# Optimization experiments

Hardware: AMD Instinct MI355X
Metric: run time of the kernel (lower is better)

The kernel has to match this reference:

```python
import jax, jax.numpy as jnp
import numpy as np

GRID_SIZE = 4
ORDER = 3
NUM_BASIS = GRID_SIZE + ORDER  # 7
KNOTS = jnp.linspace(-1.0, 1.0, NUM_BASIS + ORDER + 1)  # 11 knots


def _normalise(x):
    # eval-mode with uninitialized running stats: use batch min/max
    min_val = x.min(axis=0)
    max_val = x.max(axis=0)
    width = jnp.maximum(max_val - min_val, 0.01)
    centre = 0.5 * (max_val + min_val)
    scaled = (x - centre) / (0.5 * width)
    return jnp.clip(scaled, -2.0, 2.0)


def _bspline_basis(x):
    # x: (B, I) -> basis: (B, I, NUM_BASIS), de Boor recursion vectorized over i
    xe = x[..., None]  # (B, I, 1)
    idx = jnp.arange(NUM_BASIS)
    left, right = KNOTS[idx], KNOTS[idx + 1]
    basis = ((xe >= left) & (xe < right)).astype(x.dtype)
    last = jnp.where(xe[..., 0] == KNOTS[NUM_BASIS], 1.0, basis[..., -1])
    basis = basis.at[..., -1].set(last)
    for k in range(1, ORDER + 1):
        d1 = KNOTS[idx + k] - KNOTS[idx]
        d2 = KNOTS[idx + k + 1] - KNOTS[idx + 1]
        b_next = jnp.concatenate([basis[..., 1:], jnp.zeros_like(basis[..., :1])], axis=-1)
        t1 = jnp.where(d1 > 0, (xe - KNOTS[idx]) / jnp.where(d1 > 0, d1, 1.0), 0.0) * basis
        t2 = jnp.where(d2 > 0, (KNOTS[idx + k + 1] - xe) / jnp.where(d2 > 0, d2, 1.0), 0.0) * b_next
        basis = t1 + t2
    return basis


def setup_inputs() -> dict:
    key = jax.random.key(0)
    k1, k2, k3 = jax.random.split(key, 3)
    B, I, O = 8192, 256, 256
    x = jax.random.normal(k1, (B, I), dtype=jnp.float32)
    # xavier-uniform base_weight
    bound = float(np.sqrt(6.0 / (I + O)))
    base_weight = jax.random.uniform(k2, (O, I), minval=-bound, maxval=bound, dtype=jnp.float32)
    spline_weight = jnp.ones((O, I), dtype=jnp.float32)
    spline_coeff = 0.001 * jax.random.normal(k3, (O, I, NUM_BASIS), dtype=jnp.float32)
    bias = jnp.zeros((O,), dtype=jnp.float32)
    return {"x": x, "base_weight": base_weight, "spline_weight": spline_weight,
            "spline_coeff": spline_coeff, "bias": bias}


def reference(x, base_weight, spline_weight, spline_coeff, bias):
    x_norm = _normalise(x)                          # (B, I)
    basis = _bspline_basis(x_norm)                  # (B, I, M)
    silu_x = x_norm * jax.nn.sigmoid(x_norm)        # (B, I)
    base_out = silu_x @ base_weight.T               # sum_i silu_i * W_oi -> (B, O)
    coeff_scaled = spline_coeff * spline_weight[..., None]  # (O, I, M)
    spline_out = jnp.einsum('bim,oim->bo', basis, coeff_scaled)
    return base_out + spline_out + bias[None, :]
```

## Files before the change

kernel.cpp:

```cpp
#include <hip/hip_runtime.h>
#include <hip/hip_bf16.h>

#define B_SZ 8192
#define I_SZ 256
#define O_SZ 256
#define KDIM 2048
#define BM 32
#define BN 128
#define BKT 64
#define NT 32

typedef __bf16 bf16x8 __attribute__((ext_vector_type(8)));
typedef float f32x4 __attribute__((ext_vector_type(4)));

__global__ __launch_bounds__(256) void minmax_partial(
    const float* __restrict__ x, float* __restrict__ pmin,
    float* __restrict__ pmax) {
  const int cg = threadIdx.x & 63;
  const int rs = threadIdx.x >> 6;
  const int r0 = blockIdx.x * 64;
  const float* p = x + (size_t)(r0 + rs) * I_SZ + cg * 4;
  float4 mn = {1e30f, 1e30f, 1e30f, 1e30f};
  float4 mx = {-1e30f, -1e30f, -1e30f, -1e30f};
#pragma unroll
  for (int k = 0; k < 16; ++k) {
    const float4 v = *reinterpret_cast<const float4*>(p + (size_t)k * 4 * I_SZ);
    mn.x = fminf(mn.x, v.x); mn.y = fminf(mn.y, v.y);
    mn.z = fminf(mn.z, v.z); mn.w = fminf(mn.w, v.w);
    mx.x = fmaxf(mx.x, v.x); mx.y = fmaxf(mx.y, v.y);
    mx.z = fmaxf(mx.z, v.z); mx.w = fmaxf(mx.w, v.w);
  }
  __shared__ float rmn[4][I_SZ], rmx[4][I_SZ];
  *reinterpret_cast<float4*>(&rmn[rs][cg * 4]) = mn;
  *reinterpret_cast<float4*>(&rmx[rs][cg * 4]) = mx;
  __syncthreads();
  if (threadIdx.x < 64) {
    float4 a, b;
    const int c0 = threadIdx.x * 4;
    a.x = fminf(fminf(rmn[0][c0+0], rmn[1][c0+0]), fminf(rmn[2][c0+0], rmn[3][c0+0]));
    a.y = fminf(fminf(rmn[0][c0+1], rmn[1][c0+1]), fminf(rmn[2][c0+1], rmn[3][c0+1]));
    a.z = fminf(fminf(rmn[0][c0+2], rmn[1][c0+2]), fminf(rmn[2][c0+2], rmn[3][c0+2]));
    a.w = fminf(fminf(rmn[0][c0+3], rmn[1][c0+3]), fminf(rmn[2][c0+3], rmn[3][c0+3]));
    b.x = fmaxf(fmaxf(rmx[0][c0+0], rmx[1][c0+0]), fmaxf(rmx[2][c0+0], rmx[3][c0+0]));
    b.y = fmaxf(fmaxf(rmx[0][c0+1], rmx[1][c0+1]), fmaxf(rmx[2][c0+1], rmx[3][c0+1]));
    b.z = fmaxf(fmaxf(rmx[0][c0+2], rmx[1][c0+2]), fmaxf(rmx[2][c0+2], rmx[3][c0+2]));
    b.w = fmaxf(fmaxf(rmx[0][c0+3], rmx[1][c0+3]), fmaxf(rmx[2][c0+3], rmx[3][c0+3]));
    *reinterpret_cast<float4*>(&pmin[blockIdx.x * I_SZ + c0]) = a;
    *reinterpret_cast<float4*>(&pmax[blockIdx.x * I_SZ + c0]) = b;
  }
}

__global__ void pack_W(const float* __restrict__ bw,
                       const float* __restrict__ sw,
                       const float* __restrict__ coeff,
                       __hip_bfloat16* __restrict__ W,
                       const float* __restrict__ pmin,
                       const float* __restrict__ pmax,
                       float* __restrict__ cenrhw) {
  const int idx = blockIdx.x * blockDim.x + threadIdx.x;
  const int i = idx & (I_SZ - 1);
  const int o = idx >> 8;
  const float s = sw[idx];
  union { __hip_bfloat16 h[8]; float4 f4; } u;
#pragma unroll
  for (int m = 0; m < 7; ++m)
    u.h[m] = __float2bfloat16(coeff[(size_t)idx * 7 + m] * s);
  u.h[7] = __float2bfloat16(bw[idx]);
  const size_t off = (size_t)o * KDIM + (size_t)((i ^ (o & 7)) << 3);
  *reinterpret_cast<float4*>(&W[off]) = u.f4;

  if (blockIdx.x == 0) {
    const int c = threadIdx.x;
    float mn = 1e30f, mx = -1e30f;
#pragma unroll 8
    for (int p = 0; p < 128; ++p) {
      mn = fminf(mn, pmin[p * I_SZ + c]);
      mx = fmaxf(mx, pmax[p * I_SZ + c]);
    }
    const float width = fmaxf(mx - mn, 0.01f);
    cenrhw[2 * c]     = 0.5f * (mx + mn);
    cenrhw[2 * c + 1] = 2.0f / width;
  }
}

__device__ __forceinline__ void async16(const __hip_bfloat16* g, __hip_bfloat16* l) {
  __builtin_amdgcn_global_load_lds(
      (const __attribute__((address_space(1))) void*)g,
      (__attribute__((address_space(3))) void*)l, 16, 0, 0);
}

__global__ __launch_bounds__(256, 2) void gemm_fused(
    const float* __restrict__ x, const __hip_bfloat16* __restrict__ W,
    const float* __restrict__ cenrhw, const float* __restrict__ bias,
    float* __restrict__ out) {
  __shared__ __align__(16) __hip_bfloat16 Alds[2][BM * BKT];
  __shared__ __align__(16) __hip_bfloat16 Blds[2][BN * BKT];
  __shared__ float2 scl[I_SZ];

  const int t = threadIdx.x;
  const int lane = t & 63;
  const int wave = t >> 6;
  const int fr = lane & 15, fk = lane >> 4;

  const int bid = blockIdx.x;
  const int swz = (bid & 7) * 64 + (bid >> 3);
  const int bm = swz >> 1, bn = swz & 1;
  const int r0 = bm * BM;
  const int c0 = bn * BN;

  scl[t] = reinterpret_cast<const float2*>(cenrhw)[t];

  const int arow = t >> 3;
  const int af_  = t & 7;
  const float* xp = x + (size_t)(r0 + arow) * I_SZ + af_;

  const __hip_bfloat16* gb0 = W + (size_t)(c0 + (t >> 3)) * KDIM + (t & 7) * 8;

  f32x4 acc[2][2] = {{{0.f,0.f,0.f,0.f},{0.f,0.f,0.f,0.f}},
                     {{0.f,0.f,0.f,0.f},{0.f,0.f,0.f,0.f}}};

  auto stageB = [&](int buf, int kt) {
    const size_t k0 = (size_t)kt * BKT;
    async16(gb0 + k0,                      &Blds[buf][t * 8]);
    async16(gb0 + k0 + (size_t)32 * KDIM,  &Blds[buf][2048 + t * 8]);
    async16(gb0 + k0 + (size_t)64 * KDIM,  &Blds[buf][4096 + t * 8]);
    async16(gb0 + k0 + (size_t)96 * KDIM,  &Blds[buf][6144 + t * 8]);
  };

  auto buildA = [&](int buf, int kt, float xv) {
    const int i = kt * 8 + af_;
    const float2 s = scl[i];
    float xn = (xv - s.x) * s.y;
    xn = fminf(fmaxf(xn, -2.0f), 2.0f);
    float d[11];
#pragma unroll
    for (int j = 0; j < 11; ++j) d[j] = xn - (-1.0f + 0.2f * j);
    float bas[7];
#pragma unroll
    for (int j = 0; j < 7; ++j)
      bas[j] = (d[j] >= 0.0f && d[j + 1] < 0.0f) ? 1.0f : 0.0f;
    if (d[7] == 0.0f) bas[6] = 1.0f;
#pragma unroll
    for (int k = 1; k <= 3; ++k) {
      const float rk = (k == 1) ? 5.0f : (k == 2) ? 2.5f : (1.0f / 0.6f);
#pragma unroll
      for (int j = 0; j < 7; ++j) {
        const float bn_ = (j < 6) ? bas[j + 1] : 0.0f;
        bas[j] = (d[j] * bas[j] - d[j + k + 1] * bn_) * rk;
      }
    }
    const float silu = xn / (1.0f + __expf(-xn));
    union { __hip_bfloat16 h[8]; float4 f4; } u;
#pragma unroll
    for (int m = 0; m < 7; ++m) u.h[m] = __float2bfloat16(bas[m]);
    u.h[7] = __float2bfloat16(silu);
    const int unit = af_ ^ (arow & 7);
    *reinterpret_cast<float4*>(&Alds[buf][arow * BKT + unit * 8]) = u.f4;
  };

  auto compute = [&](int buf) {
    bf16x8 af[2][2], bg[2][2];
#pragma unroll
    for (int m = 0; m < 2; ++m)
#pragma unroll
      for (int kk = 0; kk < 2; ++kk) {
        const int row = m * 16 + fr;
        const int unit = ((kk << 2) | fk) ^ (row & 7);
        af[m][kk] = *reinterpret_cast<const bf16x8*>(&Alds[buf][row * BKT + unit * 8]);
      }
#pragma unroll
    for (int n = 0; n < 2; ++n)
#pragma unroll
      for (int kk = 0; kk < 2; ++kk) {
        const int row = wave * 32 + n * 16 + fr;
        const int unit = ((kk << 2) | fk) ^ (row & 7);
        bg[n][kk] = *reinterpret_cast<const bf16x8*>(&Blds[buf][row * BKT + unit * 8]);
      }
#pragma unroll
    for (int kk = 0; kk < 2; ++kk)
#pragma unroll
      for (int m = 0; m < 2; ++m)
#pragma unroll
        for (int n = 0; n < 2; ++n)
          acc[m][n] = __builtin_amdgcn_mfma_f32_16x16x32_bf16(
              af[m][kk], bg[n][kk], acc[m][n], 0, 0, 0);
  };

  const float xv0 = xp[0];
  float xpf = xp[8];
  __syncthreads();
  stageB(0, 0);
  buildA(0, 0, xv0);
  __syncthreads();
  int cur = 0;
  for (int kt = 0; kt < NT - 1; ++kt) {
    stageB(cur ^ 1, kt + 1);
    float xpf2 = (kt + 2 < NT) ? xp[(kt + 2) * 8] : 0.0f;
    buildA(cur ^ 1, kt + 1, xpf);
    compute(cur);
    __syncthreads();
    xpf = xpf2;
    cur ^= 1;
  }
  compute(cur);

#pragma unroll
  for (int m = 0; m < 2; ++m)
#pragma unroll
    for (int n = 0; n < 2; ++n) {
      const int col = c0 + wave * 32 + n * 16 + fr;
      const float bc = bias[col];
#pragma unroll
      for (int r = 0; r < 4; ++r) {
        const int row = r0 + m * 16 + fk * 4 + r;
        out[(size_t)row * O_SZ + col] = acc[m][n][r] + bc;
      }
    }
}

extern "C" void kernel_launch(void* const* d_in, const int* in_sizes, int n_in,
                              void* d_out, int out_size, void* d_ws, size_t ws_size,
                              hipStream_t stream) {
  const float* x     = (const float*)d_in[0];
  const float* bw    = (const float*)d_in[1];
  const float* sw    = (const float*)d_in[2];
  const float* coeff = (const float*)d_in[3];
  const float* bias  = (const float*)d_in[4];
  float* out = (float*)d_out;

  char* ws = (char*)d_ws;
  __hip_bfloat16* Wbuf = (__hip_bfloat16*)ws;
  float* pmin   = (float*)(ws + (size_t)O_SZ * KDIM * 2);
  float* pmax   = pmin + 128 * I_SZ;
  float* cenrhw = pmax + 128 * I_SZ;

  minmax_partial<<<128, 256, 0, stream>>>(x, pmin, pmax);
  pack_W<<<(O_SZ * I_SZ) / 256, 256, 0, stream>>>(bw, sw, coeff, Wbuf,
                                                  pmin, pmax, cenrhw);
  gemm_fused<<<(B_SZ / BM) * (O_SZ / BN), 256, 0, stream>>>(x, Wbuf, cenrhw,
                                                            bias, out);
}
```

Measured before the change: 47.27 us.

## Triple-buffer B tiles with partial vmcnt waits and MFMA priority boost

```diff
diff --git a/kernel.cpp b/kernel.cpp
--- a/kernel.cpp
+++ b/kernel.cpp
@@ -9,6 +9,7 @@
 #define BN 128
 #define BKT 64
 #define NT 32
+#define NPART 256
 
 typedef __bf16 bf16x8 __attribute__((ext_vector_type(8)));
 typedef float f32x4 __attribute__((ext_vector_type(4)));
@@ -18,12 +19,12 @@
     float* __restrict__ pmax) {
   const int cg = threadIdx.x & 63;
   const int rs = threadIdx.x >> 6;
-  const int r0 = blockIdx.x * 64;
+  const int r0 = blockIdx.x * 32;
   const float* p = x + (size_t)(r0 + rs) * I_SZ + cg * 4;
   float4 mn = {1e30f, 1e30f, 1e30f, 1e30f};
   float4 mx = {-1e30f, -1e30f, -1e30f, -1e30f};
 #pragma unroll
-  for (int k = 0; k < 16; ++k) {
+  for (int k = 0; k < 8; ++k) {
     const float4 v = *reinterpret_cast<const float4*>(p + (size_t)k * 4 * I_SZ);
     mn.x = fminf(mn.x, v.x); mn.y = fminf(mn.y, v.y);
     mn.z = fminf(mn.z, v.z); mn.w = fminf(mn.w, v.w);
@@ -73,7 +74,7 @@
     const int c = threadIdx.x;
     float mn = 1e30f, mx = -1e30f;
 #pragma unroll 8
-    for (int p = 0; p < 128; ++p) {
+    for (int p = 0; p < NPART; ++p) {
       mn = fminf(mn, pmin[p * I_SZ + c]);
       mx = fmaxf(mx, pmax[p * I_SZ + c]);
     }
@@ -94,7 +95,7 @@
     const float* __restrict__ cenrhw, const float* __restrict__ bias,
     float* __restrict__ out) {
   __shared__ __align__(16) __hip_bfloat16 Alds[2][BM * BKT];
-  __shared__ __align__(16) __hip_bfloat16 Blds[2][BN * BKT];
+  __shared__ __align__(16) __hip_bfloat16 Blds[3][BN * BKT];
   __shared__ float2 scl[I_SZ];
 
   const int t = threadIdx.x;
@@ -158,7 +159,7 @@
     *reinterpret_cast<float4*>(&Alds[buf][arow * BKT + unit * 8]) = u.f4;
   };
 
-  auto compute = [&](int buf) {
+  auto compute = [&](int bbuf, int abuf) {
     bf16x8 af[2][2], bg[2][2];
 #pragma unroll
     for (int m = 0; m < 2; ++m)
@@ -166,7 +167,7 @@
       for (int kk = 0; kk < 2; ++kk) {
         const int row = m * 16 + fr;
         const int unit = ((kk << 2) | fk) ^ (row & 7);
-        af[m][kk] = *reinterpret_cast<const bf16x8*>(&Alds[buf][row * BKT + unit * 8]);
+        af[m][kk] = *reinterpret_cast<const bf16x8*>(&Alds[abuf][row * BKT + unit * 8]);
       }
 #pragma unroll
     for (int n = 0; n < 2; ++n)
@@ -174,8 +175,9 @@
       for (int kk = 0; kk < 2; ++kk) {
         const int row = wave * 32 + n * 16 + fr;
         const int unit = ((kk << 2) | fk) ^ (row & 7);
-        bg[n][kk] = *reinterpret_cast<const bf16x8*>(&Blds[buf][row * BKT + unit * 8]);
-      }
+        bg[n][kk] = *reinterpret_cast<const bf16x8*>(&Blds[bbuf][row * BKT + unit * 8]);
+      }
+    __builtin_amdgcn_s_setprio(1);
 #pragma unroll
     for (int kk = 0; kk < 2; ++kk)
 #pragma unroll
@@ -184,25 +186,41 @@
         for (int n = 0; n < 2; ++n)
           acc[m][n] = __builtin_amdgcn_mfma_f32_16x16x32_bf16(
               af[m][kk], bg[n][kk], acc[m][n], 0, 0, 0);
+    __builtin_amdgcn_s_setprio(0);
   };
 
   const float xv0 = xp[0];
   float xpf = xp[8];
   __syncthreads();
   stageB(0, 0);
+  stageB(1, 1);
   buildA(0, 0, xv0);
-  __syncthreads();
-  int cur = 0;
+  asm volatile("s_waitcnt vmcnt(4) lgkmcnt(0)" ::: "memory");
+  __builtin_amdgcn_s_barrier();
+  asm volatile("" ::: "memory");
+
+  int bcur = 0;
   for (int kt = 0; kt < NT - 1; ++kt) {
-    stageB(cur ^ 1, kt + 1);
-    float xpf2 = (kt + 2 < NT) ? xp[(kt + 2) * 8] : 0.0f;
-    buildA(cur ^ 1, kt + 1, xpf);
-    compute(cur);
-    __syncthreads();
-    xpf = xpf2;
-    cur ^= 1;
-  }
-  compute(cur);
+    const int bnxt = (bcur == 2) ? 0 : bcur + 1;
+    const int bpre = (bnxt == 2) ? 0 : bnxt + 1;
+    if (kt + 2 < NT) {
+      stageB(bpre, kt + 2);
+      const float xpf2 = xp[(kt + 2) * 8];
+      buildA((kt + 1) & 1, kt + 1, xpf);
+      xpf = xpf2;
+    } else {
+      buildA((kt + 1) & 1, kt + 1, xpf);
+    }
+    compute(bcur, kt & 1);
+    if (kt < NT - 2)
+      asm volatile("s_waitcnt vmcnt(4) lgkmcnt(0)" ::: "memory");
+    else
+      asm volatile("s_waitcnt vmcnt(0) lgkmcnt(0)" ::: "memory");
+    __builtin_amdgcn_s_barrier();
+    asm volatile("" ::: "memory");
+    bcur = bnxt;
+  }
+  compute(bcur, (NT - 1) & 1);
 
 #pragma unroll
   for (int m = 0; m < 2; ++m)
@@ -231,10 +249,10 @@
   char* ws = (char*)d_ws;
   __hip_bfloat16* Wbuf = (__hip_bfloat16*)ws;
   float* pmin   = (float*)(ws + (size_t)O_SZ * KDIM * 2);
-  float* pmax   = pmin + 128 * I_SZ;
-  float* cenrhw = pmax + 128 * I_SZ;
-
-  minmax_partial<<<128, 256, 0, stream>>>(x, pmin, pmax);
+  float* pmax   = pmin + NPART * I_SZ;
+  float* cenrhw = pmax + NPART * I_SZ;
+
+  minmax_partial<<<NPART, 256, 0, stream>>>(x, pmin, pmax);
   pack_W<<<(O_SZ * I_SZ) / 256, 256, 0, stream>>>(bw, sw, coeff, Wbuf,
                                                   pmin, pmax, cenrhw);
   gemm_fused<<<(B_SZ / BM) * (O_SZ / BN), 256, 0, stream>>>(x, Wbuf, cenrhw,
```

Measured after the change: 50.28 us. 1.06x slower.
